# Performance work log

Measured on AMD Instinct MI355X. Metric: run time of the kernel, lower is better.

Reference implementation:

```python
import jax, jax.numpy as jnp
import numpy as np

B, T, V, E, H = 64, 1024, 32000, 300, 200
BUDGET = 10
L_SUP, R_SUP = -0.1, 1.1  # HardKuma stretched support


def setup_inputs() -> dict:
    key = jax.random.key(0)
    ks = jax.random.split(key, 12)
    x = jax.random.randint(ks[0], (B, T), 0, V)
    lengths = jax.random.randint(ks[1], (B,), T // 2, T + 1)
    mask = jnp.arange(T)[None, :] < lengths[:, None]  # contiguous prefix mask
    s = 1.0 / np.sqrt(H)
    return {
        "x": x,
        "mask": mask,
        "embed": jax.random.normal(ks[2], (V, E), jnp.float32) * 0.1,
        "Wih_f": jax.random.uniform(ks[3], (4 * H, E), jnp.float32, -s, s),
        "Whh_f": jax.random.uniform(ks[4], (4 * H, H), jnp.float32, -s, s),
        "b_f": jnp.zeros((4 * H,), jnp.float32),
        "Wih_b": jax.random.uniform(ks[5], (4 * H, E), jnp.float32, -s, s),
        "Whh_b": jax.random.uniform(ks[6], (4 * H, H), jnp.float32, -s, s),
        "b_b": jnp.zeros((4 * H,), jnp.float32),
        "Wa": jax.random.normal(ks[7], (1, 2 * H), jnp.float32) * 1e-3,
        "ba": jnp.zeros((1,), jnp.float32),
        "Wb": jax.random.normal(ks[8], (1, 2 * H), jnp.float32) * 1e-3,
        "bb": jnp.zeros((1,), jnp.float32),
    }


def _lstm(xs, mask, Wih, Whh, b, reverse=False):
    """Packed-sequence-equivalent (masked) unidirectional LSTM. xs:(B,T,E), mask:(B,T) bool -> (B,T,H)."""
    Bq = xs.shape[0]
    Hh = Whh.shape[1]

    def step(carry, inp):
        h, c = carry
        xt, mt = inp  # (B,E), (B,) bool
        g = xt @ Wih.T + h @ Whh.T + b  # (B,4H), torch gate order i,f,g,o
        i, f, gg, o = jnp.split(g, 4, axis=-1)
        c_new = jax.nn.sigmoid(f) * c + jax.nn.sigmoid(i) * jnp.tanh(gg)
        h_new = jax.nn.sigmoid(o) * jnp.tanh(c_new)
        m = mt[:, None]
        h = jnp.where(m, h_new, h)
        c = jnp.where(m, c_new, c)
        return (h, c), jnp.where(m, h, 0.0)  # padded outputs are zero (pack/pad behavior)

    h0 = jnp.zeros((Bq, Hh), xs.dtype)
    (_, _), ys = jax.lax.scan(step, (h0, h0), (jnp.swapaxes(xs, 0, 1), jnp.swapaxes(mask, 0, 1)), reverse=reverse)
    return jnp.swapaxes(ys, 0, 1)


def _kuma_mean(a, b):
    # E[Kuma(a,b)] = b * Beta(1 + 1/a, b), via lgamma for stability
    one_p_inv_a = 1.0 + 1.0 / a
    lbeta = jax.lax.lgamma(one_p_inv_a) + jax.lax.lgamma(b) - jax.lax.lgamma(one_p_inv_a + b)
    return b * jnp.exp(lbeta)


def _forward(x, mask, embed, Wih_f, Whh_f, b_f, Wih_b, Whh_b, b_b, Wa, ba, Wb, bb):
    maskf = mask.astype(jnp.float32)
    lengths = mask.sum(1)  # (B,)
    emb = embed[x]  # (B,T,E); dropout is identity in eval mode
    hf = _lstm(emb, mask, Wih_f, Whh_f, b_f, reverse=False)
    hb = _lstm(emb, mask, Wih_b, Whh_b, b_b, reverse=True)
    h = jnp.concatenate([hf, hb], axis=-1)  # (B,T,2H)
    hs = h / 0.01
    a = jnp.clip(jax.nn.softplus(hs @ Wa.T + ba), 1e-6, 100.0)  # (B,T,1)
    bk = jnp.clip(jax.nn.softplus(hs @ Wb.T + bb), 1e-6, 100.0)
    # HardKuma mean: stretch Kuma mean to support then rectify to [0,1]
    mean = jnp.clip(L_SUP + (R_SUP - L_SUP) * _kuma_mean(a, bk), 0.0, 1.0)
    z_probs = mean[..., 0] * maskf  # zero beyond each length (B,T)
    # per-example budget: k_b = round(budget/100 * len_b) (round-half-even, matches torch.round)
    k = jnp.round((BUDGET / 100.0) * lengths.astype(jnp.float32)).astype(jnp.int32)
    # batched variable-k top-k: rank each position by descending prob, keep rank < k
    order = jnp.argsort(-z_probs, axis=1)
    ranks = jnp.argsort(order, axis=1)  # rank of each position (0 = largest)
    sel = (ranks < k[:, None]) & (z_probs > 0)  # matches z_probs>0 after scatter-zeroing
    z = sel.astype(jnp.float32)
    return jnp.where(mask, z, 0.0)


def reference(x, mask, embed, Wih_f, Whh_f, b_f, Wih_b, Whh_b, b_b, Wa, ba, Wb, bb):
    return _forward(x, mask, embed, Wih_f, Whh_f, b_f, Wih_b, Whh_b, b_b, Wa, ba, Wb, bb)
```

## Files before the change

### kernel.cpp

```cpp
#include <hip/hip_runtime.h>
#include <math.h>

#define Bsz 64
#define Tsz 1024
#define Esz 300
#define Hsz 200
#define Gsz 800
#define NTOK (Bsz*Tsz)
#define WPAD 6400

#define FMA4(A_, W_, H_) do { \
  (A_).x = fmaf((W_).x, (H_), (A_).x); \
  (A_).y = fmaf((W_).y, (H_), (A_).y); \
  (A_).z = fmaf((W_).z, (H_), (A_).z); \
  (A_).w = fmaf((W_).w, (H_), (A_).w); } while (0)


__global__ __launch_bounds__(256) void k_lengths(const void* __restrict__ mraw,
                                                 int* __restrict__ lens) {
  __shared__ int red[256];
  const unsigned char* mb = (const unsigned char*)mraw;
  const int isbool = (mb[1] != 0);
  int b = blockIdx.x, tid = threadIdx.x;
  int s = 0;
  if (isbool) {
    const unsigned char* row = mb + (size_t)b * Tsz;
    for (int i = tid; i < Tsz; i += 256) s += (row[i] != 0);
  } else {
    const int* row = (const int*)mraw + (size_t)b * Tsz;
    for (int i = tid; i < Tsz; i += 256) s += (row[i] != 0);
  }
  red[tid] = s; __syncthreads();
  for (int off = 128; off; off >>= 1) {
    if (tid < off) red[tid] += red[tid + off];
    __syncthreads();
  }
  if (tid == 0) lens[b] = red[0];
}

__global__ __launch_bounds__(256) void k_transpose(const float* __restrict__ Whh,
                                                   float* __restrict__ WhhT) {
  int idx = blockIdx.x * 256 + threadIdx.x;
  if (idx >= Gsz * Hsz) return;
  int r = idx / Hsz, j = idx - r * Hsz;
  int rp = 4 * (r % Hsz) + r / Hsz;
  WhhT[(size_t)j * Gsz + rp] = Whh[idx];
}

#define BM 64
#define BN 160
#define BK 20
__global__ __launch_bounds__(256) void k_gemm(const int* __restrict__ x,
                                              const float* __restrict__ embed,
                                              const float* __restrict__ Wf,
                                              const float* __restrict__ biasf,
                                              const float* __restrict__ Wb_,
                                              const float* __restrict__ biasb,
                                              float* __restrict__ Pf,
                                              float* __restrict__ Pb,
                                              int t0f, int t0b, int tcShift) {
  __shared__ __align__(16) float As[BK][BM];
  __shared__ __align__(16) float Bs[BK][BN];
  __shared__ int toks[BM];
  const int revz = blockIdx.z;
  const float* __restrict__ W    = revz ? Wb_  : Wf;
  const float* __restrict__ bias = revz ? biasb : biasf;
  float* __restrict__ P          = revz ? Pb   : Pf;
  const int t0                   = revz ? t0b  : t0f;
  int tid = threadIdx.x;
  int n0 = blockIdx.x * BM;
  int j0 = blockIdx.y * BN;
  if (tid < BM) {
    int n = n0 + tid;
    int bb = n >> tcShift;
    int tl = n & ((1 << tcShift) - 1);
    toks[tid] = x[(bb << 10) + t0 + tl];
  }
  float acc[8][5];
#pragma unroll
  for (int i = 0; i < 8; i++)
#pragma unroll
    for (int j = 0; j < 5; j++) acc[i][j] = 0.f;
  int rg = tid >> 5;
  int cg = tid & 31;
  for (int k0 = 0; k0 < Esz; k0 += BK) {
    __syncthreads();
    for (int idx = tid; idx < BM * 5; idx += 256) {
      int r = idx / 5, q = idx % 5;
      const float4 v = *reinterpret_cast<const float4*>(
          embed + (size_t)toks[r] * Esz + k0 + q * 4);
      As[q * 4 + 0][r] = v.x; As[q * 4 + 1][r] = v.y;
      As[q * 4 + 2][r] = v.z; As[q * 4 + 3][r] = v.w;
    }
    for (int idx = tid; idx < BN * 5; idx += 256) {
      int j = idx / 5, q = idx % 5;
      int colg = j0 + j;
      int srcRow = (colg & 3) * Hsz + (colg >> 2);
      const float4 v = *reinterpret_cast<const float4*>(
          W + (size_t)srcRow * Esz + k0 + q * 4);
      Bs[q * 4 + 0][j] = v.x; Bs[q * 4 + 1][j] = v.y;
      Bs[q * 4 + 2][j] = v.z; Bs[q * 4 + 3][j] = v.w;
    }
    __syncthreads();
#pragma unroll
    for (int kk = 0; kk < BK; ++kk) {
      float4 a0 = *reinterpret_cast<const float4*>(&As[kk][rg * 8]);
      float4 a1 = *reinterpret_cast<const float4*>(&As[kk][rg * 8 + 4]);
      float a[8] = {a0.x, a0.y, a0.z, a0.w, a1.x, a1.y, a1.z, a1.w};
      float bv[5];
#pragma unroll
      for (int j = 0; j < 5; j++) bv[j] = Bs[kk][cg + 32 * j];
#pragma unroll
      for (int i = 0; i < 8; i++)
#pragma unroll
        for (int j = 0; j < 5; j++) acc[i][j] = fmaf(a[i], bv[j], acc[i][j]);
    }
  }
#pragma unroll
  for (int j = 0; j < 5; j++) {
    int col = j0 + cg + 32 * j;
    float bb = bias[(col & 3) * Hsz + (col >> 2)];
#pragma unroll
    for (int i = 0; i < 8; i++) {
      int n = n0 + rg * 8 + i;
      P[(size_t)n * Gsz + col] = acc[i][j] + bb;
    }
  }
}

__global__ __launch_bounds__(512, 2) void k_lstm(
    const float* __restrict__ Pf, const float* __restrict__ Pb,
    const float* __restrict__ WhhTf, const float* __restrict__ WhhTb,
    const int* __restrict__ lens,
    const float* __restrict__ Wa, const float* __restrict__ Wb,
    float* __restrict__ hcF, float* __restrict__ hcB,
    float* __restrict__ zaf, float* __restrict__ zbf,
    float* __restrict__ zab, float* __restrict__ zbb,
    int t0f, int t0b, int TC, int init) {
  __shared__ __align__(16) float h[Hsz];
  __shared__ __align__(16) float4 part[1000];
  __shared__ __align__(16) float4 wlds[8500];
  __shared__ float redA[2][8], redB[2][8];
  int bid = blockIdx.x, tid = threadIdx.x;
  int rev = bid >> 6;
  int b = bid & 63;
  int len = lens[b];
  const float* P    = rev ? Pb : Pf;
  const float* WhhT = rev ? WhhTb : WhhTf;
  float* hcb = (rev ? hcB : hcF) + (size_t)b * 2 * Hsz;
  float* za  = rev ? zab : zaf;
  float* zb  = rev ? zbb : zbf;
  int t0 = rev ? t0b : t0f;
  float wa = 0.f, wb = 0.f, c0 = 0.f;
  if (tid < Hsz) {
    h[tid] = init ? 0.f : hcb[tid];
    c0     = init ? 0.f : hcb[Hsz + tid];
    int off = rev ? Hsz : 0;
    wa = Wa[off + tid]; wb = Wb[off + tid];
  }
  const int worker = (tid < 500);
  int col = 0, gk = 0;
  if (worker) { col = tid % 100; gk = tid / 100; }
  const int hbase = gk * 40;
  const float4* __restrict__ wp4 =
      reinterpret_cast<const float4*>(WhhT) + (size_t)hbase * 200 + 2 * col;

  float4 wreg[40];
  if (worker) {
#pragma unroll
    for (int q = 0; q < 40; q++) wreg[q] = wp4[(q >> 1) * 200 + (q & 1)];
#pragma unroll
    for (int i = 0; i < 17; i++)
      wlds[i * 500 + tid] = wp4[((40 + i) >> 1) * 200 + ((40 + i) & 1)];
  }
  __syncthreads();

  int lo = t0;
  int hi = t0 + TC; if (len < hi) hi = len;
  int nsteps = hi - lo; if (nsteps < 0) nsteps = 0;

  for (int s = 0; s < nsteps; ++s) {
    int t = rev ? (hi - 1 - s) : (lo + s);
    const float4* __restrict__ Prow4 = reinterpret_cast<const float4*>(
        P + ((size_t)b * TC + (t - t0)) * Gsz);
    if (worker) {
      float4 rbuf[8];
#pragma unroll
      for (int q = 0; q < 8; q++)
        rbuf[q] = wp4[((57 + q) >> 1) * 200 + ((57 + q) & 1)];
      float4 acc0, acc1;
      if (gk == 0) { acc0 = Prow4[2 * col]; acc1 = Prow4[2 * col + 1]; }
      else {
        acc0.x = acc0.y = acc0.z = acc0.w = 0.f;
        acc1.x = acc1.y = acc1.z = acc1.w = 0.f;
      }
#pragma unroll
      for (int u = 0; u < 20; u++) {
        float hj = h[hbase + u];
        FMA4(acc0, wreg[2 * u], hj);
        FMA4(acc1, wreg[2 * u + 1], hj);
      }
#pragma unroll
      for (int i = 0; i < 17; i++) {
        float hj = h[hbase + 20 + (i >> 1)];
        float4 wv = wlds[i * 500 + tid];
        if (i & 1) { FMA4(acc1, wv, hj); } else { FMA4(acc0, wv, hj); }
      }
#pragma unroll
      for (int q = 0; q < 15; q++) {
        float4 wv = rbuf[q & 7];
        rbuf[q & 7] = wp4[((65 + q) >> 1) * 200 + ((65 + q) & 1)];
        float hj = h[hbase + ((57 + q) >> 1)];
        if ((57 + q) & 1) { FMA4(acc1, wv, hj); } else { FMA4(acc0, wv, hj); }
      }
#pragma unroll
      for (int q = 15; q < 23; q++) {
        float4 wv = rbuf[q & 7];
        float hj = h[hbase + ((57 + q) >> 1)];
        if ((57 + q) & 1) { FMA4(acc1, wv, hj); } else { FMA4(acc0, wv, hj); }
      }
      part[gk * 200 + 2 * col]     = acc0;
      part[gk * 200 + 2 * col + 1] = acc1;
    }
    __syncthreads();
    float pa = 0.f, pb = 0.f;
    if (tid < Hsz) {
      float4 p0 = part[tid],       p1 = part[200 + tid], p2 = part[400 + tid];
      float4 p3 = part[600 + tid], p4 = part[800 + tid];
      float gi = p0.x + p1.x + p2.x + p3.x + p4.x;
      float gf = p0.y + p1.y + p2.y + p3.y + p4.y;
      float gc = p0.z + p1.z + p2.z + p3.z + p4.z;
      float go = p0.w + p1.w + p2.w + p3.w + p4.w;
      float ig = 1.f / (1.f + expf(-gi));
      float fg = 1.f / (1.f + expf(-gf));
      float gt = tanhf(gc);
      float og = 1.f / (1.f + expf(-go));
      float cn = fmaf(fg, c0, ig * gt);
      float hn = og * tanhf(cn);
      c0 = cn; h[tid] = hn;
      pa = hn * wa; pb = hn * wb;
    }
#pragma unroll
    for (int off = 32; off; off >>= 1) {
      pa += __shfl_down(pa, off);
      pb += __shfl_down(pb, off);
    }
    if ((tid & 63) == 0) { redA[s & 1][tid >> 6] = pa; redB[s & 1][tid >> 6] = pb; }
    __syncthreads();
    if (tid == 0) {
      float sa = 0.f, sb = 0.f;
#pragma unroll
      for (int w = 0; w < 8; ++w) { sa += redA[s & 1][w]; sb += redB[s & 1][w]; }
      za[(size_t)b * Tsz + t] = sa;
      zb[(size_t)b * Tsz + t] = sb;
    }
  }
  if (tid < Hsz) { hcb[tid] = h[tid]; hcb[Hsz + tid] = c0; }
}

__global__ __launch_bounds__(256) void k_head(const float* __restrict__ zaf,
                                              const float* __restrict__ zbf,
                                              const float* __restrict__ zab,
                                              const float* __restrict__ zbb,
                                              const int* __restrict__ lens,
                                              const float* __restrict__ ba,
                                              const float* __restrict__ bb,
                                              float* __restrict__ zp) {
  int n = blockIdx.x * 256 + threadIdx.x;
  if (n >= NTOK) return;
  int b = n >> 10, t = n & 1023;
  if (t >= lens[b]) { zp[n] = 0.f; return; }
  double av = ((double)zaf[n] + (double)zab[n]) * 100.0 + (double)ba[0];
  double bv = ((double)zbf[n] + (double)zbb[n]) * 100.0 + (double)bb[0];
  double a  = av > 0.0 ? av + log1p(exp(-av)) : log1p(exp(av));
  double bk = bv > 0.0 ? bv + log1p(exp(-bv)) : log1p(exp(bv));
  a  = fmin(fmax(a, 1e-6), 100.0);
  bk = fmin(fmax(bk, 1e-6), 100.0);
  double ia = 1.0 + 1.0 / a;
  double lb = lgamma(ia) + lgamma(bk) - lgamma(ia + bk);
  double mean = bk * exp(lb);
  mean = -0.1 + 1.2 * mean;
  mean = fmin(fmax(mean, 0.0), 1.0);
  zp[n] = (float)mean;
}

__global__ __launch_bounds__(256) void k_select(const float* __restrict__ zp,
                                                const int* __restrict__ lens,
                                                float* __restrict__ out) {
  __shared__ float zv[Tsz];
  __shared__ float wbv[4];
  __shared__ int wbi[4];
  __shared__ int stop;
  int b = blockIdx.x, tid = threadIdx.x;
  const float* row = zp + (size_t)b * Tsz;
  for (int i = tid; i < Tsz; i += 256) zv[i] = row[i];
  if (tid == 0) stop = 0;
  int len = lens[b];
  int k = (int)rintf(0.1f * (float)len);
  __syncthreads();
  for (int it = 0; it < k; ++it) {
    float bvl = -1.f; int bil = 0;
#pragma unroll
    for (int s = 0; s < 4; s++) {
      int i = tid * 4 + s;
      float v = zv[i];
      if (v > bvl) { bvl = v; bil = i; }
    }
    for (int off = 32; off; off >>= 1) {
      float ov = __shfl_down(bvl, off);
      int   oi = __shfl_down(bil, off);
      if (ov > bvl || (ov == bvl && oi < bil)) { bvl = ov; bil = oi; }
    }
    int w = tid >> 6;
    if ((tid & 63) == 0) { wbv[w] = bvl; wbi[w] = bil; }
    __syncthreads();
    if (tid == 0) {
      float fb = wbv[0]; int fi = wbi[0];
      for (int q = 1; q < 4; q++)
        if (wbv[q] > fb || (wbv[q] == fb && wbi[q] < fi)) { fb = wbv[q]; fi = wbi[q]; }
      if (fb <= 0.f) stop = 1;
      else { out[(size_t)b * Tsz + fi] = 1.0f; zv[fi] = -1e30f; }
    }
    __syncthreads();
    if (stop) break;
  }
}

extern "C" void kernel_launch(void* const* d_in, const int* in_sizes, int n_in,
                              void* d_out, int out_size, void* d_ws, size_t ws_size,
                              hipStream_t stream) {
  const int*   x      = (const int*)d_in[0];
  const void*  mask   = d_in[1];
  const float* embed  = (const float*)d_in[2];
  const float* Wih_f  = (const float*)d_in[3];
  const float* Whh_f  = (const float*)d_in[4];
  const float* b_f    = (const float*)d_in[5];
  const float* Wih_b  = (const float*)d_in[6];
  const float* Whh_b  = (const float*)d_in[7];
  const float* b_b    = (const float*)d_in[8];
  const float* Wa     = (const float*)d_in[9];
  const float* ba     = (const float*)d_in[10];
  const float* Wb     = (const float*)d_in[11];
  const float* bb     = (const float*)d_in[12];
  float* out = (float*)d_out;

  size_t fixedBytes = (5 * (size_t)NTOK + 2 * (size_t)Bsz * 2 * Hsz +
                       2 * ((size_t)Hsz * Gsz + WPAD)) * sizeof(float) +
                      Bsz * sizeof(int) + 1024;
  int TC = 16;
  const int cand[7] = {1024, 512, 256, 128, 64, 32, 16};
  for (int i = 0; i < 7; i++) {
    size_t need = fixedBytes + 2 * (size_t)Bsz * cand[i] * Gsz * sizeof(float);
    if (need <= ws_size) { TC = cand[i]; break; }
  }
  int tcShift = 31 - __builtin_clz((unsigned)TC);

  float* Pf    = (float*)d_ws;
  float* Pb    = Pf + (size_t)Bsz * TC * Gsz;
  float* zaf   = Pb + (size_t)Bsz * TC * Gsz;
  float* zbf   = zaf + NTOK;
  float* zab   = zbf + NTOK;
  float* zbb   = zab + NTOK;
  float* zp    = zbb + NTOK;
  float* hcF   = zp + NTOK;
  float* hcB   = hcF + (size_t)Bsz * 2 * Hsz;
  float* WhhTf = hcB + (size_t)Bsz * 2 * Hsz;
  float* WhhTb = WhhTf + (size_t)Hsz * Gsz + WPAD;
  int*   lens  = (int*)(WhhTb + (size_t)Hsz * Gsz + WPAD);

  k_lengths<<<Bsz, 256, 0, stream>>>(mask, lens);

  const int tgrid = (Gsz * Hsz + 255) / 256;
  k_transpose<<<tgrid, 256, 0, stream>>>(Whh_f, WhhTf);
  k_transpose<<<tgrid, 256, 0, stream>>>(Whh_b, WhhTb);

  int nch = Tsz / TC;
  dim3 gg((Bsz * TC) / BM, Gsz / BN, 2);
  for (int ci = 0; ci < nch; ++ci) {
    int t0f = ci * TC;
    int t0b = (nch - 1 - ci) * TC;
    k_gemm<<<gg, 256, 0, stream>>>(x, embed, Wih_f, b_f, Wih_b, b_b,
                                   Pf, Pb, t0f, t0b, tcShift);
    k_lstm<<<2 * Bsz, 512, 0, stream>>>(Pf, Pb, WhhTf, WhhTb, lens, Wa, Wb,
                                        hcF, hcB, zaf, zbf, zab, zbb,
                                        t0f, t0b, TC, ci == 0);
  }

  k_head<<<NTOK / 256, 256, 0, stream>>>(zaf, zbf, zab, zbb, lens, ba, bb, zp);

  (void)hipMemsetAsync(d_out, 0, (size_t)out_size * sizeof(float), stream);
  k_select<<<Bsz, 256, 0, stream>>>(zp, lens, out);
}
```

Baseline: 4.268 ms.

## Overlap next chunk's input GEMM with LSTM recurrence in one fused launch

Fuses the input-projection GEMM for the next time chunk into the LSTM kernel as extra blocks. The 128 recurrent blocks keep running the serial scan while the other blocks fill the second buffer of a double-buffered gate workspace. This is meant to hide GEMM time behind the latency-bound recurrence, which otherwise leaves most CUs idle. It also fixes the chunk size at 256 and moves one more weight slice into LDS. The cost is four chunk buffers of workspace, with a fallback to the serial path, and GEMM blocks that may compete with the LSTM blocks for CU resources.

Measured after the change: 3.588 ms. 15.9% less time.

```diff
diff --git a/kernel.cpp b/kernel.cpp
--- a/kernel.cpp
+++ b/kernel.cpp
@@ -72,9 +72,7 @@
   int j0 = blockIdx.y * BN;
   if (tid < BM) {
     int n = n0 + tid;
-    int bb = n >> tcShift;
-    int tl = n & ((1 << tcShift) - 1);
-    toks[tid] = x[(bb << 10) + t0 + tl];
+    toks[tid] = x[((n >> tcShift) << 10) + t0 + (n & ((1 << tcShift) - 1))];
   }
   float acc[8][5];
 #pragma unroll
@@ -128,7 +126,8 @@
   }
 }
 
-__global__ __launch_bounds__(512, 2) void k_lstm(
+#define BM2 128
+__global__ __launch_bounds__(512, 2) void k_fused(
     const float* __restrict__ Pf, const float* __restrict__ Pb,
     const float* __restrict__ WhhTf, const float* __restrict__ WhhTb,
     const int* __restrict__ lens,
@@ -136,12 +135,91 @@
     float* __restrict__ hcF, float* __restrict__ hcB,
     float* __restrict__ zaf, float* __restrict__ zbf,
     float* __restrict__ zab, float* __restrict__ zbb,
-    int t0f, int t0b, int TC, int init) {
+    int t0f, int t0b, int TC, int tcShift, int init,
+    const int* __restrict__ x, const float* __restrict__ embed,
+    const float* __restrict__ Wihf, const float* __restrict__ bf,
+    const float* __restrict__ Wihb, const float* __restrict__ bb_,
+    float* __restrict__ PfN, float* __restrict__ PbN,
+    int t0fN, int t0bN, int gemmValid) {
   __shared__ __align__(16) float h[Hsz];
   __shared__ __align__(16) float4 part[1000];
-  __shared__ __align__(16) float4 wlds[8500];
+  __shared__ __align__(16) float4 wlds[9000];
   __shared__ float redA[2][8], redB[2][8];
   int bid = blockIdx.x, tid = threadIdx.x;
+
+  if (bid >= 128) {
+    if (!gemmValid) return;
+    float* As = reinterpret_cast<float*>(wlds);
+    float* Bs = As + BK * BM2;
+    int*  toks = reinterpret_cast<int*>(Bs + BK * BN);
+    int gid = bid - 128;
+    int dir = gid / 640;
+    int rem = gid - dir * 640;
+    int gy = rem / 128;
+    int gx = rem - gy * 128;
+    const float* __restrict__ W    = dir ? Wihb : Wihf;
+    const float* __restrict__ bias = dir ? bb_  : bf;
+    float* __restrict__ P          = dir ? PbN  : PfN;
+    const int t0                   = dir ? t0bN : t0fN;
+    int n0 = gx * BM2;
+    int j0 = gy * BN;
+    if (tid < BM2) {
+      int n = n0 + tid;
+      toks[tid] = x[((n >> tcShift) << 10) + t0 + (n & ((1 << tcShift) - 1))];
+    }
+    float acc[8][5];
+#pragma unroll
+    for (int i = 0; i < 8; i++)
+#pragma unroll
+      for (int j = 0; j < 5; j++) acc[i][j] = 0.f;
+    int rg = tid >> 5;
+    int cg = tid & 31;
+    for (int k0 = 0; k0 < Esz; k0 += BK) {
+      __syncthreads();
+      for (int idx = tid; idx < BM2 * 5; idx += 512) {
+        int r = idx / 5, q = idx % 5;
+        const float4 v = *reinterpret_cast<const float4*>(
+            embed + (size_t)toks[r] * Esz + k0 + q * 4);
+        As[(q * 4 + 0) * BM2 + r] = v.x; As[(q * 4 + 1) * BM2 + r] = v.y;
+        As[(q * 4 + 2) * BM2 + r] = v.z; As[(q * 4 + 3) * BM2 + r] = v.w;
+      }
+      for (int idx = tid; idx < BN * 5; idx += 512) {
+        int j = idx / 5, q = idx % 5;
+        int colg = j0 + j;
+        int srcRow = (colg & 3) * Hsz + (colg >> 2);
+        const float4 v = *reinterpret_cast<const float4*>(
+            W + (size_t)srcRow * Esz + k0 + q * 4);
+        Bs[(q * 4 + 0) * BN + j] = v.x; Bs[(q * 4 + 1) * BN + j] = v.y;
+        Bs[(q * 4 + 2) * BN + j] = v.z; Bs[(q * 4 + 3) * BN + j] = v.w;
+      }
+      __syncthreads();
+#pragma unroll
+      for (int kk = 0; kk < BK; ++kk) {
+        float4 a0 = *reinterpret_cast<const float4*>(&As[kk * BM2 + rg * 8]);
+        float4 a1 = *reinterpret_cast<const float4*>(&As[kk * BM2 + rg * 8 + 4]);
+        float a[8] = {a0.x, a0.y, a0.z, a0.w, a1.x, a1.y, a1.z, a1.w};
+        float bv[5];
+#pragma unroll
+        for (int j = 0; j < 5; j++) bv[j] = Bs[kk * BN + cg + 32 * j];
+#pragma unroll
+        for (int i = 0; i < 8; i++)
+#pragma unroll
+          for (int j = 0; j < 5; j++) acc[i][j] = fmaf(a[i], bv[j], acc[i][j]);
+      }
+    }
+#pragma unroll
+    for (int j = 0; j < 5; j++) {
+      int col = j0 + cg + 32 * j;
+      float bb = bias[(col & 3) * Hsz + (col >> 2)];
+#pragma unroll
+      for (int i = 0; i < 8; i++) {
+        int n = n0 + rg * 8 + i;
+        P[(size_t)n * Gsz + col] = acc[i][j] + bb;
+      }
+    }
+    return;
+  }
+
   int rev = bid >> 6;
   int b = bid & 63;
   int len = lens[b];
@@ -170,7 +248,7 @@
 #pragma unroll
     for (int q = 0; q < 40; q++) wreg[q] = wp4[(q >> 1) * 200 + (q & 1)];
 #pragma unroll
-    for (int i = 0; i < 17; i++)
+    for (int i = 0; i < 18; i++)
       wlds[i * 500 + tid] = wp4[((40 + i) >> 1) * 200 + ((40 + i) & 1)];
   }
   __syncthreads();
@@ -187,7 +265,7 @@
       float4 rbuf[8];
 #pragma unroll
       for (int q = 0; q < 8; q++)
-        rbuf[q] = wp4[((57 + q) >> 1) * 200 + ((57 + q) & 1)];
+        rbuf[q] = wp4[((58 + q) >> 1) * 200 + ((58 + q) & 1)];
       float4 acc0, acc1;
       if (gk == 0) { acc0 = Prow4[2 * col]; acc1 = Prow4[2 * col + 1]; }
       else {
@@ -201,23 +279,23 @@
         FMA4(acc1, wreg[2 * u + 1], hj);
       }
 #pragma unroll
-      for (int i = 0; i < 17; i++) {
+      for (int i = 0; i < 18; i++) {
         float hj = h[hbase + 20 + (i >> 1)];
         float4 wv = wlds[i * 500 + tid];
         if (i & 1) { FMA4(acc1, wv, hj); } else { FMA4(acc0, wv, hj); }
       }
 #pragma unroll
-      for (int q = 0; q < 15; q++) {
+      for (int q = 0; q < 14; q++) {
         float4 wv = rbuf[q & 7];
-        rbuf[q & 7] = wp4[((65 + q) >> 1) * 200 + ((65 + q) & 1)];
-        float hj = h[hbase + ((57 + q) >> 1)];
-        if ((57 + q) & 1) { FMA4(acc1, wv, hj); } else { FMA4(acc0, wv, hj); }
-      }
-#pragma unroll
-      for (int q = 15; q < 23; q++) {
+        rbuf[q & 7] = wp4[((66 + q) >> 1) * 200 + ((66 + q) & 1)];
+        float hj = h[hbase + ((58 + q) >> 1)];
+        if ((58 + q) & 1) { FMA4(acc1, wv, hj); } else { FMA4(acc0, wv, hj); }
+      }
+#pragma unroll
+      for (int q = 14; q < 22; q++) {
         float4 wv = rbuf[q & 7];
-        float hj = h[hbase + ((57 + q) >> 1)];
-        if ((57 + q) & 1) { FMA4(acc1, wv, hj); } else { FMA4(acc0, wv, hj); }
+        float hj = h[hbase + ((58 + q) >> 1)];
+        if ((58 + q) & 1) { FMA4(acc1, wv, hj); } else { FMA4(acc0, wv, hj); }
       }
       part[gk * 200 + 2 * col]     = acc0;
       part[gk * 200 + 2 * col + 1] = acc1;
@@ -347,17 +425,34 @@
   size_t fixedBytes = (5 * (size_t)NTOK + 2 * (size_t)Bsz * 2 * Hsz +
                        2 * ((size_t)Hsz * Gsz + WPAD)) * sizeof(float) +
                       Bsz * sizeof(int) + 1024;
-  int TC = 16;
-  const int cand[7] = {1024, 512, 256, 128, 64, 32, 16};
-  for (int i = 0; i < 7; i++) {
-    size_t need = fixedBytes + 2 * (size_t)Bsz * cand[i] * Gsz * sizeof(float);
-    if (need <= ws_size) { TC = cand[i]; break; }
-  }
-  int tcShift = 31 - __builtin_clz((unsigned)TC);
-
-  float* Pf    = (float*)d_ws;
-  float* Pb    = Pf + (size_t)Bsz * TC * Gsz;
-  float* zaf   = Pb + (size_t)Bsz * TC * Gsz;
+  const int TCo = 256;
+  size_t chunkFlO = (size_t)Bsz * TCo * Gsz;
+  size_t needOverlap = fixedBytes + 4 * chunkFlO * sizeof(float);
+  int overlap = (ws_size >= needOverlap);
+
+  int TC = TCo, tcShift = 8, nP = 4;
+  if (!overlap) {
+    const int cand[5] = {256, 128, 64, 32, 16};
+    for (int i = 0; i < 5; i++) {
+      size_t need = fixedBytes + 2 * (size_t)Bsz * cand[i] * Gsz * sizeof(float);
+      if (need <= ws_size) { TC = cand[i]; break; }
+    }
+    tcShift = 31 - __builtin_clz((unsigned)TC);
+    nP = 2;
+  }
+  size_t chunkFl = (size_t)Bsz * TC * Gsz;
+
+  float* Pbase = (float*)d_ws;
+  float* PfA[2], *PbA[2];
+  if (overlap) {
+    PfA[0] = Pbase;               PfA[1] = Pbase + chunkFl;
+    PbA[0] = Pbase + 2 * chunkFl; PbA[1] = Pbase + 3 * chunkFl;
+  } else {
+    PfA[0] = PfA[1] = Pbase;
+    PbA[0] = PbA[1] = Pbase + chunkFl;
+  }
+  float* rest  = Pbase + nP * chunkFl;
+  float* zaf   = rest;
   float* zbf   = zaf + NTOK;
   float* zab   = zbf + NTOK;
   float* zbb   = zab + NTOK;
@@ -369,21 +464,36 @@
   int*   lens  = (int*)(WhhTb + (size_t)Hsz * Gsz + WPAD);
 
   k_lengths<<<Bsz, 256, 0, stream>>>(mask, lens);
-
   const int tgrid = (Gsz * Hsz + 255) / 256;
   k_transpose<<<tgrid, 256, 0, stream>>>(Whh_f, WhhTf);
   k_transpose<<<tgrid, 256, 0, stream>>>(Whh_b, WhhTb);
 
   int nch = Tsz / TC;
-  dim3 gg((Bsz * TC) / BM, Gsz / BN, 2);
-  for (int ci = 0; ci < nch; ++ci) {
-    int t0f = ci * TC;
-    int t0b = (nch - 1 - ci) * TC;
+  if (overlap) {
+    dim3 gg((Bsz * TC) / BM, Gsz / BN, 2);
     k_gemm<<<gg, 256, 0, stream>>>(x, embed, Wih_f, b_f, Wih_b, b_b,
-                                   Pf, Pb, t0f, t0b, tcShift);
-    k_lstm<<<2 * Bsz, 512, 0, stream>>>(Pf, Pb, WhhTf, WhhTb, lens, Wa, Wb,
-                                        hcF, hcB, zaf, zbf, zab, zbb,
-                                        t0f, t0b, TC, ci == 0);
+                                   PfA[0], PbA[0], 0, (nch - 1) * TC, tcShift);
+    for (int i = 0; i < nch; ++i) {
+      int gv = (i < nch - 1);
+      int grid = 128 + (gv ? 1280 : 0);
+      k_fused<<<grid, 512, 0, stream>>>(
+          PfA[i & 1], PbA[i & 1], WhhTf, WhhTb, lens, Wa, Wb, hcF, hcB,
+          zaf, zbf, zab, zbb, i * TC, (nch - 1 - i) * TC, TC, tcShift, i == 0,
+          x, embed, Wih_f, b_f, Wih_b, b_b,
+          PfA[(i + 1) & 1], PbA[(i + 1) & 1],
+          (i + 1) * TC, (nch - 2 - i) * TC, gv);
+    }
+  } else {
+    dim3 gg((Bsz * TC) / BM, Gsz / BN, 2);
+    for (int i = 0; i < nch; ++i) {
+      k_gemm<<<gg, 256, 0, stream>>>(x, embed, Wih_f, b_f, Wih_b, b_b,
+                                     PfA[0], PbA[0], i * TC,
+                                     (nch - 1 - i) * TC, tcShift);
+      k_fused<<<128, 512, 0, stream>>>(
+          PfA[0], PbA[0], WhhTf, WhhTb, lens, Wa, Wb, hcF, hcB,
+          zaf, zbf, zab, zbb, i * TC, (nch - 1 - i) * TC, TC, tcShift, i == 0,
+          x, embed, Wih_f, b_f, Wih_b, b_b, PfA[0], PbA[0], 0, 0, 0);
+    }
   }
 
   k_head<<<NTOK / 256, 256, 0, stream>>>(zaf, zbf, zab, zbb, lens, ba, bb, zp);
```
